# Kernel tuning notes

Measured on AMD Instinct MI355X. Metric: run time of the kernel, lower is better.

## Reference

```python
import jax, jax.numpy as jnp
import numpy as np

INITIAL_DELTA = 0.1
DELTA_LOW = 0.02
DELTA_HIGH = 0.1
SCAN_LEN_OFFSET = 20  # scan over num_columns - 20
EXTRA_LO, EXTRA_HI = 232, 252  # pass-through columns


def setup_inputs() -> dict:
    key = jax.random.key(0)
    x = jax.random.normal(key, (128, 1024, 252), dtype=jnp.float32)
    return {"x": x}


def _delta_modulate(x):
    # x: [B, R, C]; scan over first C-20 columns with per-(b,r) state.
    B, R, C = x.shape
    n_steps = C - SCAN_LEN_OFFSET
    xs = jnp.moveaxis(x[:, :, :n_steps], -1, 0)  # [n_steps, B, R]

    dc0 = jnp.zeros((B, R), dtype=x.dtype)
    delta0 = jnp.full((B, R), INITIAL_DELTA, dtype=x.dtype)
    tc0 = jnp.zeros((B, R), dtype=x.dtype)
    ntc0 = jnp.zeros((B, R), dtype=x.dtype)

    def step(carry, x_i):
        dc, delta, tc, ntc = carry
        up = x_i > (dc + delta)
        dn = x_i < (dc - delta)
        trig = up | dn
        tc = jnp.where(trig, tc + 1.0, 0.0)
        ntc = jnp.where(trig, 0.0, ntc + 1.0)
        delta = jnp.where(tc >= 3.0, DELTA_LOW, delta)
        delta = jnp.where(ntc >= 3.0, DELTA_HIGH, delta)
        dc = jnp.where(trig, x_i, dc)
        return (dc, delta, tc, ntc), (up, dn)

    _, (UP, DN) = jax.lax.scan(step, (dc0, delta0, tc0, ntc0), xs)
    # UP/DN: [n_steps, B, R] bool -> [B, R, n_steps]
    UP = jnp.moveaxis(UP, 0, -1)
    DN = jnp.moveaxis(DN, 0, -1)
    encoded = jnp.concatenate([UP, DN], axis=-1).astype(jnp.float32)
    extra = x[:, :, EXTRA_LO:EXTRA_HI]
    return jnp.concatenate([encoded, extra], axis=-1).astype(jnp.float32)


def reference(x) -> jnp.ndarray:
    return _delta_modulate(x)
```

## Files before the change

kernel.cpp:

```cpp
#include <hip/hip_runtime.h>

#define CC 252
#define NSTEPS 232
#define OUTC 484
#define NROWS (128 * 1024)

#define INITIAL_DELTA 0.1f
#define DELTA_LOW 0.02f
#define DELTA_HIGH 0.1f

__device__ __forceinline__ void step1(float xi, unsigned& upbit, unsigned& dnbit,
                                      float& dc, float& delta, float& tc, float& ntc)
{
    bool up = xi > dc + delta;
    bool dn = xi < dc - delta;
    bool trig = up || dn;
    tc  = trig ? tc + 1.0f : 0.0f;
    ntc = trig ? 0.0f : ntc + 1.0f;
    delta = (tc  >= 3.0f) ? DELTA_LOW  : delta;
    delta = (ntc >= 3.0f) ? DELTA_HIGH : delta;
    dc = trig ? xi : dc;
    upbit = up ? 1u : 0u;
    dnbit = dn ? 1u : 0u;
}

__device__ __forceinline__ float bitf(const unsigned* w, int b)
{
    return ((w[b >> 5] >> (b & 31)) & 1u) ? 1.0f : 0.0f;
}

__global__ __launch_bounds__(256) void DeltaModulator_kernel(
    const float* __restrict__ x, float* __restrict__ out)
{
    const int row = blockIdx.x * blockDim.x + threadIdx.x;
    if (row >= NROWS) return;

    const float* xrow = x + (size_t)row * CC;
    const float4* __restrict__ x4 = reinterpret_cast<const float4*>(xrow);

    float dc = 0.0f, delta = INITIAL_DELTA, tc = 0.0f, ntc = 0.0f;

    unsigned up_w[8], dn_w[8];

    #pragma unroll
    for (int ch = 0; ch < 7; ++ch) {
        float4 xv[8];
        #pragma unroll
        for (int k = 0; k < 8; ++k) xv[k] = x4[ch * 8 + k];
        unsigned uw = 0u, dw = 0u;
        #pragma unroll
        for (int k = 0; k < 8; ++k) {
            float xs[4] = {xv[k].x, xv[k].y, xv[k].z, xv[k].w};
            #pragma unroll
            for (int j = 0; j < 4; ++j) {
                unsigned ub, db;
                step1(xs[j], ub, db, dc, delta, tc, ntc);
                uw |= ub << (k * 4 + j);
                dw |= db << (k * 4 + j);
            }
        }
        up_w[ch] = uw;
        dn_w[ch] = dw;
    }
    {
        float4 xv[2];
        #pragma unroll
        for (int k = 0; k < 2; ++k) xv[k] = x4[56 + k];
        unsigned uw = 0u, dw = 0u;
        #pragma unroll
        for (int k = 0; k < 2; ++k) {
            float xs[4] = {xv[k].x, xv[k].y, xv[k].z, xv[k].w};
            #pragma unroll
            for (int j = 0; j < 4; ++j) {
                unsigned ub, db;
                step1(xs[j], ub, db, dc, delta, tc, ntc);
                uw |= ub << (k * 4 + j);
                dw |= db << (k * 4 + j);
            }
        }
        up_w[7] = uw;
        dn_w[7] = dw;
    }

    const float4* __restrict__ xe = reinterpret_cast<const float4*>(xrow + NSTEPS);
    float4 ev[5];
    #pragma unroll
    for (int i = 0; i < 5; ++i) ev[i] = xe[i];

    float4* __restrict__ o4 = reinterpret_cast<float4*>(out + (size_t)row * OUTC);

    #pragma unroll
    for (int f = 0; f < 58; ++f) {
        const int b = 4 * f;
        o4[f] = make_float4(bitf(up_w, b), bitf(up_w, b + 1),
                            bitf(up_w, b + 2), bitf(up_w, b + 3));
    }
    #pragma unroll
    for (int f = 0; f < 58; ++f) {
        const int b = 4 * f;
        o4[58 + f] = make_float4(bitf(dn_w, b), bitf(dn_w, b + 1),
                                 bitf(dn_w, b + 2), bitf(dn_w, b + 3));
    }
    #pragma unroll
    for (int i = 0; i < 5; ++i) o4[116 + i] = ev[i];
}

extern "C" void kernel_launch(void* const* d_in, const int* in_sizes, int n_in,
                              void* d_out, int out_size, void* d_ws, size_t ws_size,
                              hipStream_t stream) {
    const float* x = (const float*)d_in[0];
    float* out = (float*)d_out;
    const int threads = 256;
    const int blocks = (NROWS + threads - 1) / threads;
    DeltaModulator_kernel<<<blocks, threads, 0, stream>>>(x, out);
}
```

Measured before the change: 445.2 us.

## Stage scan bits in LDS and write output rows cooperatively coalesced

Each thread still runs the sequential scan for one row, but it now stores its packed up/down bit words and the pass-through columns into shared memory instead of writing its own output row directly. After a barrier, the block writes its 256 output rows as one contiguous region, with threads striding through float4 slots. Before this, each thread wrote a separate row whose stride is 1936 bytes, so stores within a wavefront were uncoalesced. The cost is extra LDS traffic, a __syncthreads, and index arithmetic in the store loop.

Measured after the change: 359.2 us. 1.24x faster.

```diff
diff --git a/kernel.cpp b/kernel.cpp
--- a/kernel.cpp
+++ b/kernel.cpp
@@ -4,105 +4,127 @@
 #define NSTEPS 232
 #define OUTC 484
 #define NROWS (128 * 1024)
+#define ROWS_PER_BLOCK 256
 
 #define INITIAL_DELTA 0.1f
 #define DELTA_LOW 0.02f
 #define DELTA_HIGH 0.1f
 
-__device__ __forceinline__ void step1(float xi, unsigned& upbit, unsigned& dnbit,
-                                      float& dc, float& delta, float& tc, float& ntc)
-{
-    bool up = xi > dc + delta;
-    bool dn = xi < dc - delta;
-    bool trig = up || dn;
-    tc  = trig ? tc + 1.0f : 0.0f;
-    ntc = trig ? 0.0f : ntc + 1.0f;
-    delta = (tc  >= 3.0f) ? DELTA_LOW  : delta;
-    delta = (ntc >= 3.0f) ? DELTA_HIGH : delta;
-    dc = trig ? xi : dc;
-    upbit = up ? 1u : 0u;
-    dnbit = dn ? 1u : 0u;
-}
-
-__device__ __forceinline__ float bitf(const unsigned* w, int b)
-{
-    return ((w[b >> 5] >> (b & 31)) & 1u) ? 1.0f : 0.0f;
-}
+#define BITS_STRIDE 17
+#define EXTRA_STRIDE 21
 
 __global__ __launch_bounds__(256) void DeltaModulator_kernel(
     const float* __restrict__ x, float* __restrict__ out)
 {
-    const int row = blockIdx.x * blockDim.x + threadIdx.x;
-    if (row >= NROWS) return;
+    __shared__ unsigned bits_lds[ROWS_PER_BLOCK * BITS_STRIDE];
+    __shared__ float    extra_lds[ROWS_PER_BLOCK * EXTRA_STRIDE];
 
-    const float* xrow = x + (size_t)row * CC;
-    const float4* __restrict__ x4 = reinterpret_cast<const float4*>(xrow);
+    const int t = threadIdx.x;
+    const int row0 = blockIdx.x * ROWS_PER_BLOCK;
 
-    float dc = 0.0f, delta = INITIAL_DELTA, tc = 0.0f, ntc = 0.0f;
+    {
+        const int row = row0 + t;
+        const float* xrow = x + (size_t)row * CC;
+        const float4* __restrict__ x4 = reinterpret_cast<const float4*>(xrow);
 
-    unsigned up_w[8], dn_w[8];
+        float dc = 0.0f, delta = INITIAL_DELTA, tc = 0.0f, ntc = 0.0f;
+        unsigned* __restrict__ myb = &bits_lds[t * BITS_STRIDE];
 
-    #pragma unroll
-    for (int ch = 0; ch < 7; ++ch) {
-        float4 xv[8];
         #pragma unroll
-        for (int k = 0; k < 8; ++k) xv[k] = x4[ch * 8 + k];
-        unsigned uw = 0u, dw = 0u;
-        #pragma unroll
-        for (int k = 0; k < 8; ++k) {
-            float xs[4] = {xv[k].x, xv[k].y, xv[k].z, xv[k].w};
+        for (int ch = 0; ch < 7; ++ch) {
+            float4 xv[8];
             #pragma unroll
-            for (int j = 0; j < 4; ++j) {
-                unsigned ub, db;
-                step1(xs[j], ub, db, dc, delta, tc, ntc);
-                uw |= ub << (k * 4 + j);
-                dw |= db << (k * 4 + j);
+            for (int k = 0; k < 8; ++k) xv[k] = x4[ch * 8 + k];
+            unsigned uw = 0u, dw = 0u;
+            #pragma unroll
+            for (int k = 0; k < 8; ++k) {
+                float xs[4] = {xv[k].x, xv[k].y, xv[k].z, xv[k].w};
+                #pragma unroll
+                for (int j = 0; j < 4; ++j) {
+                    float xi = xs[j];
+                    bool up = xi > dc + delta;
+                    bool dn = xi < dc - delta;
+                    bool trig = up || dn;
+                    tc  = trig ? tc + 1.0f : 0.0f;
+                    ntc = trig ? 0.0f : ntc + 1.0f;
+                    delta = (tc  >= 3.0f) ? DELTA_LOW  : delta;
+                    delta = (ntc >= 3.0f) ? DELTA_HIGH : delta;
+                    dc = trig ? xi : dc;
+                    uw |= (up ? 1u : 0u) << (k * 4 + j);
+                    dw |= (dn ? 1u : 0u) << (k * 4 + j);
+                }
+            }
+            myb[ch]     = uw;
+            myb[8 + ch] = dw;
+        }
+        {
+            float4 xv[2];
+            #pragma unroll
+            for (int k = 0; k < 2; ++k) xv[k] = x4[56 + k];
+            unsigned uw = 0u, dw = 0u;
+            #pragma unroll
+            for (int k = 0; k < 2; ++k) {
+                float xs[4] = {xv[k].x, xv[k].y, xv[k].z, xv[k].w};
+                #pragma unroll
+                for (int j = 0; j < 4; ++j) {
+                    float xi = xs[j];
+                    bool up = xi > dc + delta;
+                    bool dn = xi < dc - delta;
+                    bool trig = up || dn;
+                    tc  = trig ? tc + 1.0f : 0.0f;
+                    ntc = trig ? 0.0f : ntc + 1.0f;
+                    delta = (tc  >= 3.0f) ? DELTA_LOW  : delta;
+                    delta = (ntc >= 3.0f) ? DELTA_HIGH : delta;
+                    dc = trig ? xi : dc;
+                    uw |= (up ? 1u : 0u) << (k * 4 + j);
+                    dw |= (dn ? 1u : 0u) << (k * 4 + j);
+                }
+            }
+            myb[7]  = uw;
+            myb[15] = dw;
+        }
+        {
+            const float4* __restrict__ xe = reinterpret_cast<const float4*>(xrow + NSTEPS);
+            float* __restrict__ mye = &extra_lds[t * EXTRA_STRIDE];
+            #pragma unroll
+            for (int i = 0; i < 5; ++i) {
+                float4 v = xe[i];
+                mye[i * 4 + 0] = v.x;
+                mye[i * 4 + 1] = v.y;
+                mye[i * 4 + 2] = v.z;
+                mye[i * 4 + 3] = v.w;
             }
         }
-        up_w[ch] = uw;
-        dn_w[ch] = dw;
-    }
-    {
-        float4 xv[2];
-        #pragma unroll
-        for (int k = 0; k < 2; ++k) xv[k] = x4[56 + k];
-        unsigned uw = 0u, dw = 0u;
-        #pragma unroll
-        for (int k = 0; k < 2; ++k) {
-            float xs[4] = {xv[k].x, xv[k].y, xv[k].z, xv[k].w};
-            #pragma unroll
-            for (int j = 0; j < 4; ++j) {
-                unsigned ub, db;
-                step1(xs[j], ub, db, dc, delta, tc, ntc);
-                uw |= ub << (k * 4 + j);
-                dw |= db << (k * 4 + j);
-            }
-        }
-        up_w[7] = uw;
-        dn_w[7] = dw;
     }
 
-    const float4* __restrict__ xe = reinterpret_cast<const float4*>(xrow + NSTEPS);
-    float4 ev[5];
-    #pragma unroll
-    for (int i = 0; i < 5; ++i) ev[i] = xe[i];
+    __syncthreads();
 
-    float4* __restrict__ o4 = reinterpret_cast<float4*>(out + (size_t)row * OUTC);
+    float4* __restrict__ o4 = reinterpret_cast<float4*>(out + (size_t)row0 * OUTC);
 
-    #pragma unroll
-    for (int f = 0; f < 58; ++f) {
-        const int b = 4 * f;
-        o4[f] = make_float4(bitf(up_w, b), bitf(up_w, b + 1),
-                            bitf(up_w, b + 2), bitf(up_w, b + 3));
+    int r = (t >= 242) ? 2 : ((t >= 121) ? 1 : 0);
+    int f = t - r * 121;
+
+    #pragma unroll 1
+    for (int i = 0; i < 121; ++i) {
+        float4 v;
+        if (f < 116) {
+            const int idx   = (f < 58) ? f : f - 58;
+            const int wbase = (f < 58) ? 0 : 8;
+            const unsigned word = bits_lds[r * BITS_STRIDE + wbase + (idx >> 3)];
+            const int s = 4 * (idx & 7);
+            v = make_float4((float)((word >> s) & 1u),
+                            (float)((word >> (s + 1)) & 1u),
+                            (float)((word >> (s + 2)) & 1u),
+                            (float)((word >> (s + 3)) & 1u));
+        } else {
+            const float* e = &extra_lds[r * EXTRA_STRIDE + (f - 116) * 4];
+            v = make_float4(e[0], e[1], e[2], e[3]);
+        }
+        o4[r * 121 + f] = v;
+
+        f += 14; r += 2;
+        if (f >= 121) { f -= 121; r += 1; }
     }
-    #pragma unroll
-    for (int f = 0; f < 58; ++f) {
-        const int b = 4 * f;
-        o4[58 + f] = make_float4(bitf(dn_w, b), bitf(dn_w, b + 1),
-                                 bitf(dn_w, b + 2), bitf(dn_w, b + 3));
-    }
-    #pragma unroll
-    for (int i = 0; i < 5; ++i) o4[116 + i] = ev[i];
 }
 
 extern "C" void kernel_launch(void* const* d_in, const int* in_sizes, int n_in,
@@ -111,6 +133,6 @@
     const float* x = (const float*)d_in[0];
     float* out = (float*)d_out;
     const int threads = 256;
-    const int blocks = (NROWS + threads - 1) / threads;
+    const int blocks = NROWS / ROWS_PER_BLOCK;
     DeltaModulator_kernel<<<blocks, threads, 0, stream>>>(x, out);
 }
```
